# Kernel optimization log

Hardware: AMD Instinct MI355X
Metric: run time of the kernel (lower is better)

Reference implementation:

```python
import jax, jax.numpy as jnp
import numpy as np

DIM = 2048
NHEADS = 32
HEAD_DIM = DIM // NHEADS
EPS = 1e-6


def _rmsnorm(t):
    # RMSNorm over last dim, no weight
    return t * jax.lax.rsqrt(jnp.mean(t * t, axis=-1, keepdims=True) + EPS)


def setup_inputs() -> dict:
    key = jax.random.key(0)
    kx, kc, kq, kk, kv = jax.random.split(key, 5)
    x = jax.random.normal(kx, (2, 4096, DIM), dtype=jnp.float32)
    context = jax.random.normal(kc, (2, 512, DIM), dtype=jnp.float32)
    std = 0.02
    Wq = jax.random.normal(kq, (DIM, DIM), dtype=jnp.float32) * std
    Wk = jax.random.normal(kk, (DIM, DIM), dtype=jnp.float32) * std
    Wv = jax.random.normal(kv, (DIM, DIM), dtype=jnp.float32) * std
    return {"x": x, "context": context, "Wq": Wq, "Wk": Wk, "Wv": Wv}


def reference(x, context, Wq, Wk, Wv):
    b, n, _ = x.shape
    m = context.shape[1]
    # projections (torch Linear: y = x @ W.T, no bias)
    q = x @ Wq.T                      # (b, n, dim)
    k_raw = context @ Wk.T            # (b, m, dim)
    v_raw = context @ Wv.T            # (b, m, dim)

    # split q into heads: b n (h d) -> b h n d
    q = q.reshape(b, n, NHEADS, HEAD_DIM).transpose(0, 2, 1, 3)

    # faithful to the original: cat(k,v) then 'b n (h d j)' with j=2
    kv = jnp.concatenate([k_raw, v_raw], axis=-1)          # (b, m, 2*dim)
    kv = kv.reshape(b, m, NHEADS, HEAD_DIM, 2)             # (h d j) factorization
    k = kv[..., 0].transpose(0, 2, 1, 3)                   # (b, h, m, d)
    v = kv[..., 1].transpose(0, 2, 1, 3)                   # (b, h, m, d)

    # per-head QK RMSNorm (no weight)
    q = _rmsnorm(q)
    k = _rmsnorm(k)

    scale = HEAD_DIM ** -0.5
    scores = jnp.einsum('bhnd,bhmd->bhnm', q, k) * scale
    attn = jax.nn.softmax(scores, axis=-1)
    out = jnp.einsum('bhnm,bhmd->bhnd', attn, v)           # (b, h, n, d)
    # back to (b, n, dim)
    return out.transpose(0, 2, 1, 3).reshape(b, n, NHEADS * HEAD_DIM)
```

## Files before the change

### kernel.cpp

```cpp
#include <hip/hip_runtime.h>
#include <cstdint>


typedef unsigned short u16;
typedef unsigned int u32;
typedef __bf16 bf16x8 __attribute__((ext_vector_type(8)));
typedef float f32x4 __attribute__((ext_vector_type(4)));
typedef float f32x16 __attribute__((ext_vector_type(16)));

__device__ __forceinline__ u16 f2bf(float f) {
  union { float f; unsigned u; } a; a.f = f;
  unsigned r = a.u + 0x7FFFu + ((a.u >> 16) & 1u);
  return (u16)(r >> 16);
}

__device__ __forceinline__ void gload_lds16(const u16* g, u16* l) {
  __builtin_amdgcn_global_load_lds((const __attribute__((address_space(1))) void*)g,
                                   (__attribute__((address_space(3))) void*)l, 16, 0, 0);
}

__global__ __launch_bounds__(256) void cvt_bf16(const float4* __restrict__ in,
                                                uint2* __restrict__ out, int n4) {
  int i = blockIdx.x * 256 + threadIdx.x;
  if (i >= n4) return;
  float4 v = in[i];
  uint2 o;
  o.x = (unsigned)f2bf(v.x) | ((unsigned)f2bf(v.y) << 16);
  o.y = (unsigned)f2bf(v.z) | ((unsigned)f2bf(v.w) << 16);
  out[i] = o;
}

template <bool QNORM>
__global__ __launch_bounds__(256) void gemm_bt(const u16* __restrict__ A,
                                               const u16* __restrict__ B,
                                               float* __restrict__ C,
                                               u16* __restrict__ QN, int ldc) {
  constexpr int K = 2048;
  __shared__ __align__(16) u16 As[128 * 32];
  __shared__ __align__(16) u16 Bs[128 * 32];
  const int t = threadIdx.x;
  const int w = t >> 6, l = t & 63;
  const int wr = w >> 1, wc = w & 1;
  const int lr = l & 15, lg = l >> 4;
  const int brow = blockIdx.x << 7, bcol = blockIdx.y << 7;

  f32x4 acc[4][4] = {};

  const int c0 = (w << 6) + l;
  const u16* Ab = A + (size_t)brow * K;
  const u16* Bb = B + (size_t)bcol * K;

  for (int kt = 0; kt < K; kt += 32) {
    __syncthreads();
#pragma unroll
    for (int i = 0; i < 2; ++i) {
      const int c = (i << 8) + c0;
      const int row = c >> 2, koff = (c & 3) << 3;
      gload_lds16(Ab + (size_t)row * K + kt + koff, As + (((i << 8) + (w << 6)) << 3));
      gload_lds16(Bb + (size_t)row * K + kt + koff, Bs + (((i << 8) + (w << 6)) << 3));
    }
    __syncthreads();
    bf16x8 af[4], bfr[4];
#pragma unroll
    for (int mi = 0; mi < 4; ++mi)
      af[mi] = *(const bf16x8*)&As[(((wr << 6) + (mi << 4) + lr) << 5) + (lg << 3)];
#pragma unroll
    for (int ni = 0; ni < 4; ++ni)
      bfr[ni] = *(const bf16x8*)&Bs[(((wc << 6) + (ni << 4) + lr) << 5) + (lg << 3)];
#pragma unroll
    for (int mi = 0; mi < 4; ++mi)
#pragma unroll
      for (int ni = 0; ni < 4; ++ni)
        acc[mi][ni] = __builtin_amdgcn_mfma_f32_16x16x32_bf16(af[mi], bfr[ni], acc[mi][ni], 0, 0, 0);
  }

  if (QNORM) {
    const int head = (bcol + (wc << 6)) >> 6;
#pragma unroll
    for (int mi = 0; mi < 4; ++mi) {
#pragma unroll
      for (int r = 0; r < 4; ++r) {
        float ss = 0.f;
#pragma unroll
        for (int ni = 0; ni < 4; ++ni) { float v = acc[mi][ni][r]; ss += v * v; }
        ss += __shfl_xor(ss, 1); ss += __shfl_xor(ss, 2);
        ss += __shfl_xor(ss, 4); ss += __shfl_xor(ss, 8);
        const float sc = rsqrtf(ss * (1.f / 64.f) + 1e-6f) * (0.125f * 1.4426950408889634f);
        const int row = brow + (wr << 6) + (mi << 4) + (lg << 2) + r;
        const int b = row >> 12, n = row & 4095;
        u16* o = QN + ((size_t)((b << 5) + head) * 4096 + n) * 64;
#pragma unroll
        for (int ni = 0; ni < 4; ++ni)
          o[(ni << 4) + lr] = f2bf(acc[mi][ni][r] * sc);
      }
    }
  } else {
#pragma unroll
    for (int mi = 0; mi < 4; ++mi)
#pragma unroll
      for (int r = 0; r < 4; ++r) {
        const int row = brow + (wr << 6) + (mi << 4) + (lg << 2) + r;
        float* o = C + (size_t)row * ldc + bcol + (wc << 6);
#pragma unroll
        for (int ni = 0; ni < 4; ++ni)
          o[(ni << 4) + lr] = acc[mi][ni][r];
      }
  }
}

__global__ __launch_bounds__(256) void kvbuild2(const float* __restrict__ kv,
                                                u16* __restrict__ kn,
                                                u16* __restrict__ vtn) {
  __shared__ u16 Vl[64][72];
  const int t = threadIdx.x;
  const int bh = blockIdx.x >> 3, mt = blockIdx.x & 7;
  const int b = bh >> 5, h = bh & 31;
  const int mloc = t >> 2, dc = (t & 3) << 4;
  const int m = (mt << 6) + mloc;
  const float2* src = (const float2*)(kv + ((size_t)((b << 9) + m)) * 4096 + ((h >> 4) << 11))
                      + ((h & 15) << 6) + dc;
  float kvals[16], vvals[16];
  float ss = 0.f;
#pragma unroll
  for (int dd = 0; dd < 16; ++dd) {
    float2 p = src[dd];
    kvals[dd] = p.x; vvals[dd] = p.y;
    ss += p.x * p.x;
  }
  ss += __shfl_xor(ss, 1); ss += __shfl_xor(ss, 2);
  const float sc = rsqrtf(ss * (1.f / 64.f) + 1e-6f);
  union { uint4 u4[2]; u16 h[16]; } ko;
#pragma unroll
  for (int dd = 0; dd < 16; ++dd) ko.h[dd] = f2bf(kvals[dd] * sc);
  u16* kdst = kn + ((size_t)bh * 512 + m) * 64 + dc;
  *(uint4*)kdst = ko.u4[0];
  *(uint4*)(kdst + 8) = ko.u4[1];
#pragma unroll
  for (int dd = 0; dd < 16; ++dd) Vl[dc + dd][mloc] = f2bf(vvals[dd]);
  __syncthreads();
  const int drow = t >> 2, mc = (t & 3) << 4;
  uint4 r0 = *(const uint4*)&Vl[drow][mc];
  uint4 r1 = *(const uint4*)&Vl[drow][mc + 8];
  u16* vdst = vtn + ((size_t)(bh << 6) + drow) * 512 + (mt << 6) + mc;
  *(uint4*)vdst = r0;
  *(uint4*)(vdst + 8) = r1;
}

__global__ __launch_bounds__(256) void attn2(const u16* __restrict__ qn,
                                             const u16* __restrict__ kn,
                                             const u16* __restrict__ vtn,
                                             float* __restrict__ out) {
  __shared__ __align__(16) u16 Kt[64 * 72];
  __shared__ __align__(16) u16 Vt[64 * 72];
  const int t = threadIdx.x, w = t >> 6, l = t & 63;
  const int i31 = l & 31, hi = l >> 5;
  const int nblk = blockIdx.x, bh = blockIdx.y;
  const int b = bh >> 5, h = bh & 31;
  const int qrow = (nblk << 7) + (w << 5) + i31;

  const u16* qb = qn + ((size_t)bh * 4096 + qrow) * 64 + (hi << 3);
  bf16x8 bq[4];
#pragma unroll
  for (int kt = 0; kt < 4; ++kt) bq[kt] = *(const bf16x8*)(qb + (kt << 4));

  f32x16 po[2];
#pragma unroll
  for (int d = 0; d < 2; ++d)
#pragma unroll
    for (int r = 0; r < 16; ++r) po[d][r] = 0.f;
  float mrun = -3e38f, lrun = 0.f;

  const u16* kb = kn + ((size_t)bh << 9) * 64;
  const u16* vb = vtn + ((size_t)bh << 6) * 512;
  const int srow = t >> 2, sp = (t & 3) << 3;

  for (int mt = 0; mt < 8; ++mt) {
    __syncthreads();
    {
      const u16* gk = kb + (size_t)((mt << 6) + srow) * 64 + sp;
      uint4 a0 = *(const uint4*)gk;
      uint4 a1 = *(const uint4*)(gk + 32);
      const u16* gv = vb + (size_t)srow * 512 + (mt << 6) + sp;
      uint4 b0 = *(const uint4*)gv;
      uint4 b1 = *(const uint4*)(gv + 32);
      *(uint4*)&Kt[srow * 72 + sp] = a0;
      *(uint4*)&Kt[srow * 72 + sp + 32] = a1;
      *(uint4*)&Vt[srow * 72 + sp] = b0;
      *(uint4*)&Vt[srow * 72 + sp + 32] = b1;
    }
    __syncthreads();

    f32x16 fs[2];
#pragma unroll
    for (int jt = 0; jt < 2; ++jt) {
      f32x16 s = {};
#pragma unroll
      for (int kt = 0; kt < 4; ++kt) {
        const bf16x8 ak = *(const bf16x8*)&Kt[((jt << 5) + i31) * 72 + (kt << 4) + (hi << 3)];
        s = __builtin_amdgcn_mfma_f32_32x32x16_bf16(ak, bq[kt], s, 0, 0, 0);
      }
      fs[jt] = s;
    }

    float pm = fs[0][0];
#pragma unroll
    for (int r = 1; r < 16; ++r) pm = fmaxf(pm, fs[0][r]);
#pragma unroll
    for (int r = 0; r < 16; ++r) pm = fmaxf(pm, fs[1][r]);
    pm = fmaxf(pm, __shfl_xor(pm, 32));
    if (!__all(pm <= mrun + 8.f)) {
      const float mnew = fmaxf(mrun, pm);
      const float corr = exp2f(mrun - mnew);
      lrun *= corr;
#pragma unroll
      for (int d = 0; d < 2; ++d)
#pragma unroll
        for (int r = 0; r < 16; ++r) po[d][r] *= corr;
      mrun = mnew;
    }
    float rs = 0.f;
    u32 pq[2][4][2];
#pragma unroll
    for (int jt = 0; jt < 2; ++jt)
#pragma unroll
      for (int q = 0; q < 4; ++q)
#pragma unroll
        for (int rp = 0; rp < 2; ++rp) {
          const float p0 = exp2f(fs[jt][(q << 2) + (rp << 1)] - mrun);
          const float p1 = exp2f(fs[jt][(q << 2) + (rp << 1) + 1] - mrun);
          rs += p0 + p1;
          union { u32 u; __bf16 h2[2]; } pk;
          pk.h2[0] = (__bf16)p0;
          pk.h2[1] = (__bf16)p1;
          pq[jt][q][rp] = pk.u;
        }
    rs += __shfl_xor(rs, 32);
    lrun += rs;

#pragma unroll
    for (int kk = 0; kk < 4; ++kk) {
      const int jt = kk >> 1, q0 = (kk & 1) << 1;
      union { u32 wd[4]; bf16x8 v; } pf;
#pragma unroll
      for (int rp = 0; rp < 2; ++rp) {
        const u32 v0 = pq[jt][q0][rp], v1 = pq[jt][q0 + 1][rp];
        const u32 send = hi ? v0 : v1;
        const u32 ex = (u32)__shfl_xor((int)send, 32);
        pf.wd[rp] = hi ? ex : v0;
        pf.wd[2 + rp] = hi ? v1 : ex;
      }
#pragma unroll
      for (int dt = 0; dt < 2; ++dt) {
        const bf16x8 av = *(const bf16x8*)&Vt[((dt << 5) + i31) * 72 + (kk << 4) + (hi << 3)];
        po[dt] = __builtin_amdgcn_mfma_f32_32x32x16_bf16(av, pf.v, po[dt], 0, 0, 0);
      }
    }
  }

  const float inv = 1.f / lrun;
  float* ob = out + ((size_t)(b << 12) + qrow) * 2048 + (h << 6) + (hi << 2);
#pragma unroll
  for (int dt = 0; dt < 2; ++dt)
#pragma unroll
    for (int q = 0; q < 4; ++q) {
      float4 v = { po[dt][(q << 2)] * inv, po[dt][(q << 2) + 1] * inv,
                   po[dt][(q << 2) + 2] * inv, po[dt][(q << 2) + 3] * inv };
      *(float4*)(ob + (dt << 5) + (q << 3)) = v;
    }
}

extern "C" void kernel_launch(void* const* d_in, const int* in_sizes, int n_in,
                              void* d_out, int out_size, void* d_ws, size_t ws_size,
                              hipStream_t stream) {
  const float* x   = (const float*)d_in[0];
  const float* ctx = (const float*)d_in[1];
  const float* Wq  = (const float*)d_in[2];
  const float* Wk  = (const float*)d_in[3];
  const float* Wv  = (const float*)d_in[4];
  float* out = (float*)d_out;
  char* ws = (char*)d_ws;

  u16* xb   = (u16*)(ws + 0);
  u16* cb   = (u16*)(ws + 33554432);
  u16* Wqb  = (u16*)(ws + 37748736);
  u16* Wkb  = (u16*)(ws + 46137344);
  u16* Wvb  = (u16*)(ws + 54525952);
  u16* qnp  = (u16*)(ws + 62914560);
  float* kvraw = (float*)(ws + 0);
  u16* knp  = (u16*)(ws + 16777216);
  u16* vtnp = (u16*)(ws + 20971520);

  cvt_bf16<<<16384, 256, 0, stream>>>((const float4*)x,   (uint2*)xb,  4194304);
  cvt_bf16<<<2048,  256, 0, stream>>>((const float4*)ctx, (uint2*)cb,   524288);
  cvt_bf16<<<4096,  256, 0, stream>>>((const float4*)Wq,  (uint2*)Wqb, 1048576);
  cvt_bf16<<<4096,  256, 0, stream>>>((const float4*)Wk,  (uint2*)Wkb, 1048576);
  cvt_bf16<<<4096,  256, 0, stream>>>((const float4*)Wv,  (uint2*)Wvb, 1048576);

  gemm_bt<true ><<<dim3(64, 16), 256, 0, stream>>>(xb, Wqb, nullptr, qnp, 0);
  gemm_bt<false><<<dim3(8, 32),  256, 0, stream>>>(cb, Wkb, kvraw, nullptr, 4096);
  kvbuild2<<<512, 256, 0, stream>>>(kvraw, knp, vtnp);
  attn2<<<dim3(32, 64), 256, 0, stream>>>(qnp, knp, vtnp, out);
}
```

Measured before the change: 397.7 us.

## Add 256x256 double-buffered swizzled Q-projection GEMM with fused RMSNorm epilogue

Replaces the 128x128 single-buffered Q projection GEMM with a dedicated 512-thread kernel that computes 256x256 tiles with K-step 64. It double-buffers LDS, issues its global-to-LDS loads in interleaved chunks between MFMA phases, XOR-swizzles the LDS layout to avoid bank conflicts, and raises wave priority around the MFMA blocks. The aim is higher operand reuse and overlap of memory latency with compute for the largest GEMM. In exchange it uses 128 KB of LDS per block and only 256 blocks, which limits occupancy and leaves little slack in the tail wave.

```diff
diff --git a/kernel.cpp b/kernel.cpp
--- a/kernel.cpp
+++ b/kernel.cpp
@@ -30,11 +30,144 @@
   out[i] = o;
 }
 
-template <bool QNORM>
+__global__ __launch_bounds__(512, 2) void qgemm256(const u16* __restrict__ A,
+                                                   const u16* __restrict__ B,
+                                                   u16* __restrict__ QN) {
+  constexpr int K = 2048, T = 32;
+  __shared__ __align__(16) u16 As[2][256 * 64];
+  __shared__ __align__(16) u16 Bs[2][256 * 64];
+  const int t = threadIdx.x;
+  const int wid = t >> 6, l = t & 63;
+  const int wr = wid >> 2, wc = wid & 3;
+  const int lr = l & 15, lg = l >> 4;
+  const int bid = blockIdx.x;
+  const int bx = bid >> 3, by = bid & 7;
+  const int brow = bx << 8, bcol = by << 8;
+
+  const int srcu = ((l & 7) ^ (l >> 3)) << 3;
+  const int growA = brow + (wid << 3) + (l >> 3);
+  const int growB = bcol + (wid << 3) + (l >> 3);
+
+  const int u2k0 = ((lg ^ (l & 7)) << 3);
+  const int u2k1 = u2k0 ^ 32;
+  const int rbA = (((wr << 7) + lr) << 6);
+  const int rbB = (((wc << 6) + lr) << 6);
+
+  f32x4 acc[8][4] = {};
+
+  auto stage = [&](int buf, int half, int kto, bool isB) {
+    const u16* gp = isB ? B : A;
+    const int grow = (isB ? growB : growA) + (half << 7);
+    u16* lb = (isB ? Bs[buf] : As[buf]) + (half << 13) + (wid << 9);
+#pragma unroll
+    for (int i = 0; i < 2; ++i)
+      gload_lds16(gp + (size_t)(grow + (i << 6)) * K + kto + srcu, lb + (i << 12));
+  };
+
+  stage(0, 0, 0, false); stage(0, 1, 0, false);
+  stage(0, 0, 0, true);  stage(0, 1, 0, true);
+  asm volatile("s_waitcnt vmcnt(0)" ::: "memory");
+  __builtin_amdgcn_s_barrier();
+
+  for (int tt = 0; tt < T; ++tt) {
+    const int bufc = tt & 1, bufn = bufc ^ 1;
+    const int kto = (tt + 1) << 6;
+    const bool pre = (tt + 1 < T);
+
+    if (pre) {
+      stage(bufn, 0, kto, false);
+      asm volatile("s_waitcnt vmcnt(2)" ::: "memory");
+    } else {
+      asm volatile("s_waitcnt vmcnt(0)" ::: "memory");
+    }
+    __builtin_amdgcn_sched_barrier(0);
+    __builtin_amdgcn_s_barrier();
+
+    bf16x8 bfr[4][2];
+#pragma unroll
+    for (int ni = 0; ni < 4; ++ni) {
+      bfr[ni][0] = *(const bf16x8*)&Bs[bufc][rbB + (ni << 10) + u2k0];
+      bfr[ni][1] = *(const bf16x8*)&Bs[bufc][rbB + (ni << 10) + u2k1];
+    }
+    {
+      bf16x8 af[2][2];
+#pragma unroll
+      for (int j = 0; j < 2; ++j) {
+        af[j][0] = *(const bf16x8*)&As[bufc][rbA + (j << 10) + u2k0];
+        af[j][1] = *(const bf16x8*)&As[bufc][rbA + (j << 10) + u2k1];
+      }
+      asm volatile("s_waitcnt lgkmcnt(0)" ::: "memory");
+      __builtin_amdgcn_sched_barrier(0);
+      __builtin_amdgcn_s_setprio(1);
+#pragma unroll
+      for (int j = 0; j < 2; ++j)
+#pragma unroll
+        for (int ni = 0; ni < 4; ++ni)
+#pragma unroll
+          for (int kk = 0; kk < 2; ++kk)
+            acc[j][ni] = __builtin_amdgcn_mfma_f32_16x16x32_bf16(
+                af[j][kk], bfr[ni][kk], acc[j][ni], 0, 0, 0);
+      __builtin_amdgcn_s_setprio(0);
+      __builtin_amdgcn_sched_barrier(0);
+      __builtin_amdgcn_s_barrier();
+    }
+
+#pragma unroll
+    for (int p = 1; p < 4; ++p) {
+      const int mi0 = p << 1;
+      bf16x8 af[2][2];
+#pragma unroll
+      for (int j = 0; j < 2; ++j) {
+        af[j][0] = *(const bf16x8*)&As[bufc][rbA + ((mi0 + j) << 10) + u2k0];
+        af[j][1] = *(const bf16x8*)&As[bufc][rbA + ((mi0 + j) << 10) + u2k1];
+      }
+      if (pre) {
+        if (p == 1) stage(bufn, 1, kto, false);
+        else stage(bufn, p - 2, kto, true);
+      }
+      __builtin_amdgcn_sched_barrier(0);
+      __builtin_amdgcn_s_barrier();
+      asm volatile("s_waitcnt lgkmcnt(0)" ::: "memory");
+      __builtin_amdgcn_sched_barrier(0);
+      __builtin_amdgcn_s_setprio(1);
+#pragma unroll
+      for (int j = 0; j < 2; ++j)
+#pragma unroll
+        for (int ni = 0; ni < 4; ++ni)
+#pragma unroll
+          for (int kk = 0; kk < 2; ++kk)
+            acc[mi0 + j][ni] = __builtin_amdgcn_mfma_f32_16x16x32_bf16(
+                af[j][kk], bfr[ni][kk], acc[mi0 + j][ni], 0, 0, 0);
+      __builtin_amdgcn_s_setprio(0);
+      __builtin_amdgcn_sched_barrier(0);
+      __builtin_amdgcn_s_barrier();
+    }
+  }
+
+  const int head = (by << 2) + wc;
+#pragma unroll
+  for (int mi = 0; mi < 8; ++mi) {
+#pragma unroll
+    for (int r = 0; r < 4; ++r) {
+      float ss = 0.f;
+#pragma unroll
+      for (int ni = 0; ni < 4; ++ni) { float v = acc[mi][ni][r]; ss += v * v; }
+      ss += __shfl_xor(ss, 1); ss += __shfl_xor(ss, 2);
+      ss += __shfl_xor(ss, 4); ss += __shfl_xor(ss, 8);
+      const float sc = rsqrtf(ss * (1.f / 64.f) + 1e-6f) * (0.125f * 1.4426950408889634f);
+      const int row = brow + (wr << 7) + (mi << 4) + (lg << 2) + r;
+      const int b = row >> 12, n = row & 4095;
+      u16* o = QN + ((size_t)((b << 5) + head) * 4096 + n) * 64;
+#pragma unroll
+      for (int ni = 0; ni < 4; ++ni)
+        o[(ni << 4) + lr] = f2bf(acc[mi][ni][r] * sc);
+    }
+  }
+}
+
 __global__ __launch_bounds__(256) void gemm_bt(const u16* __restrict__ A,
                                                const u16* __restrict__ B,
-                                               float* __restrict__ C,
-                                               u16* __restrict__ QN, int ldc) {
+                                               float* __restrict__ C, int ldc) {
   constexpr int K = 2048;
   __shared__ __align__(16) u16 As[128 * 32];
   __shared__ __align__(16) u16 Bs[128 * 32];
@@ -74,38 +207,16 @@
         acc[mi][ni] = __builtin_amdgcn_mfma_f32_16x16x32_bf16(af[mi], bfr[ni], acc[mi][ni], 0, 0, 0);
   }
 
-  if (QNORM) {
-    const int head = (bcol + (wc << 6)) >> 6;
-#pragma unroll
-    for (int mi = 0; mi < 4; ++mi) {
-#pragma unroll
-      for (int r = 0; r < 4; ++r) {
-        float ss = 0.f;
-#pragma unroll
-        for (int ni = 0; ni < 4; ++ni) { float v = acc[mi][ni][r]; ss += v * v; }
-        ss += __shfl_xor(ss, 1); ss += __shfl_xor(ss, 2);
-        ss += __shfl_xor(ss, 4); ss += __shfl_xor(ss, 8);
-        const float sc = rsqrtf(ss * (1.f / 64.f) + 1e-6f) * (0.125f * 1.4426950408889634f);
-        const int row = brow + (wr << 6) + (mi << 4) + (lg << 2) + r;
-        const int b = row >> 12, n = row & 4095;
-        u16* o = QN + ((size_t)((b << 5) + head) * 4096 + n) * 64;
-#pragma unroll
-        for (int ni = 0; ni < 4; ++ni)
-          o[(ni << 4) + lr] = f2bf(acc[mi][ni][r] * sc);
-      }
-    }
-  } else {
-#pragma unroll
-    for (int mi = 0; mi < 4; ++mi)
-#pragma unroll
-      for (int r = 0; r < 4; ++r) {
-        const int row = brow + (wr << 6) + (mi << 4) + (lg << 2) + r;
-        float* o = C + (size_t)row * ldc + bcol + (wc << 6);
-#pragma unroll
-        for (int ni = 0; ni < 4; ++ni)
-          o[(ni << 4) + lr] = acc[mi][ni][r];
-      }
-  }
+#pragma unroll
+  for (int mi = 0; mi < 4; ++mi)
+#pragma unroll
+    for (int r = 0; r < 4; ++r) {
+      const int row = brow + (wr << 6) + (mi << 4) + (lg << 2) + r;
+      float* o = C + (size_t)row * ldc + bcol + (wc << 6);
+#pragma unroll
+      for (int ni = 0; ni < 4; ++ni)
+        o[(ni << 4) + lr] = acc[mi][ni][r];
+    }
 }
 
 __global__ __launch_bounds__(256) void kvbuild2(const float* __restrict__ kv,
@@ -296,8 +407,8 @@
   cvt_bf16<<<4096,  256, 0, stream>>>((const float4*)Wk,  (uint2*)Wkb, 1048576);
   cvt_bf16<<<4096,  256, 0, stream>>>((const float4*)Wv,  (uint2*)Wvb, 1048576);
 
-  gemm_bt<true ><<<dim3(64, 16), 256, 0, stream>>>(xb, Wqb, nullptr, qnp, 0);
-  gemm_bt<false><<<dim3(8, 32),  256, 0, stream>>>(cb, Wkb, kvraw, nullptr, 4096);
+  qgemm256<<<256, 512, 0, stream>>>(xb, Wqb, qnp);
+  gemm_bt<<<dim3(8, 32), 256, 0, stream>>>(cb, Wkb, kvraw, 4096);
   kvbuild2<<<512, 256, 0, stream>>>(kvraw, knp, vtnp);
   attn2<<<dim3(32, 64), 256, 0, stream>>>(qnp, knp, vtnp, out);
 }
```

Measured after the change: 381.1 us. 4.2% less time.
